# Kernel optimization log

Hardware: AMD Instinct MI355X
Metric: run time of the kernel (lower is better)

## Reference

```python
import jax, jax.numpy as jnp
import numpy as np

B, S, D, H = 4, 2048, 1024, 16
HD = D // H  # head_dim = 64


def rope(x):
    # canonical interleaved RoPE over the full feature dim, applied pre-head-split
    # x: [B, S, D]
    d = x.shape[-1]
    inv_freq = 1.0 / (10000.0 ** (jnp.arange(0, d, 2, dtype=jnp.float32) / d))  # [D/2]
    pos = jnp.arange(x.shape[1], dtype=jnp.float32)
    ang = pos[:, None] * inv_freq[None, :]          # [S, D/2]
    cos, sin = jnp.cos(ang), jnp.sin(ang)
    x1, x2 = x[..., 0::2], x[..., 1::2]             # even/odd pairs
    r1 = x1 * cos - x2 * sin
    r2 = x1 * sin + x2 * cos
    return jnp.stack([r1, r2], axis=-1).reshape(x.shape)


def setup_inputs() -> dict:
    key = jax.random.key(0)
    ks = jax.random.split(key, 9)
    s = 1.0 / np.sqrt(D)
    def lin(k):
        kw, kb = jax.random.split(k)
        W = jax.random.uniform(kw, (D, D), jnp.float32, -s, s)
        b = jax.random.uniform(kb, (D,), jnp.float32, -s, s)
        return W, b
    Wq, bq = lin(ks[0]); Wk, bk = lin(ks[1]); Wv, bv = lin(ks[2]); W0, b0 = lin(ks[3])
    x = jax.random.normal(ks[4], (B, S, D), jnp.float32)
    return {"x": x, "Wq": Wq, "bq": bq, "Wk": Wk, "bk": bk,
            "Wv": Wv, "bv": bv, "W0": W0, "b0": b0}


def reference(x, Wq, bq, Wk, bk, Wv, bv, W0, b0):
    # QKV projections (torch Linear: x @ W.T + b; here W stored as [in, out])
    q = x @ Wq + bq
    k = x @ Wk + bk
    v = x @ Wv + bv
    # RoPE applied to full d_model before head split (as in the source)
    q = rope(q)
    k = rope(k)
    # split heads -> [B, H, S, HD]
    b, s, _ = x.shape
    qh = q.reshape(b, s, H, HD).transpose(0, 2, 1, 3)
    kh = k.reshape(b, s, H, HD).transpose(0, 2, 1, 3)
    vh = v.reshape(b, s, H, HD).transpose(0, 2, 1, 3)
    scores = jnp.einsum("bhqd,bhkd->bhqk", qh, kh) / jnp.sqrt(jnp.float32(HD))
    attn = jax.nn.softmax(scores, axis=-1)  # dropout p=0.0 -> identity
    out = jnp.einsum("bhqk,bhkd->bhqd", attn, vh)
    out = out.transpose(0, 2, 1, 3).reshape(b, s, D)
    return out @ W0 + b0
```

## Files before the change

### kernel.cpp

```cpp
#include <hip/hip_runtime.h>
#include <hip/hip_bf16.h>

typedef unsigned short u16;
typedef u16 u16x8 __attribute__((ext_vector_type(8)));
typedef float f32x4 __attribute__((ext_vector_type(4)));
typedef __bf16 bf16x8 __attribute__((ext_vector_type(8)));

#define B_ 4
#define S_ 2048
#define D_ 1024
#define H_ 16
#define HD_ 64
#define M_ (B_*S_)

#if __has_builtin(__builtin_amdgcn_exp2f)
#define EXP2(x) __builtin_amdgcn_exp2f(x)
#else
#define EXP2(x) exp2f(x)
#endif

__device__ __forceinline__ f32x4 MFMA(u16x8 a, u16x8 b, f32x4 c) {
  return __builtin_amdgcn_mfma_f32_16x16x32_bf16(
      __builtin_bit_cast(bf16x8, a), __builtin_bit_cast(bf16x8, b), c, 0, 0, 0);
}

__device__ __forceinline__ u16 f2b(float f) {
  return __builtin_bit_cast(u16, __float2bfloat16(f));
}

__device__ __forceinline__ void load_lds16(const void* g, void* l) {
  __builtin_amdgcn_global_load_lds(
      (const __attribute__((address_space(1))) void*)g,
      (__attribute__((address_space(3))) void*)l, 16, 0, 0);
}

__device__ __forceinline__ unsigned int cvtpk(float lo, float hi) {
  unsigned int r;
  asm("v_cvt_pk_bf16_f32 %0, %1, %2" : "=v"(r) : "v"(lo), "v"(hi));
  return r;
}

__global__ __launch_bounds__(256) void k_rope_tab(float2* __restrict__ tab) {
  int i = blockIdx.x * 256 + threadIdx.x;
  if (i >= S_ * (D_ / 2)) return;
  int s = i >> 9;
  int f = i & 511;
  float invf = (float)exp(-(double)f / 512.0 * 9.210340371976184);
  float ang = (float)s * invf;
  tab[i] = make_float2(cosf(ang), sinf(ang));
}

__global__ __launch_bounds__(256) void k_cvt(const float* __restrict__ x,
                                             u16* __restrict__ xb, int n) {
  int i = blockIdx.x * 256 + threadIdx.x;
  if (i * 4 >= n) return;
  float4 v = ((const float4*)x)[i];
  ushort4 o;
  o.x = f2b(v.x); o.y = f2b(v.y); o.z = f2b(v.z); o.w = f2b(v.w);
  ((ushort4*)xb)[i] = o;
}

__global__ __launch_bounds__(256) void k_transpose4(
    const float* __restrict__ Wq, const float* __restrict__ Wk,
    const float* __restrict__ Wv, const float* __restrict__ W0,
    u16* __restrict__ Tq, u16* __restrict__ Tk, u16* __restrict__ Tv,
    u16* __restrict__ T0) {
  const float* W = (blockIdx.z == 0) ? Wq : (blockIdx.z == 1) ? Wk
                   : (blockIdx.z == 2) ? Wv : W0;
  u16* WT = (blockIdx.z == 0) ? Tq : (blockIdx.z == 1) ? Tk
            : (blockIdx.z == 2) ? Tv : T0;
  __shared__ float t[32][33];
  int tx = threadIdx.x, ty = threadIdx.y;
  int bx = blockIdx.x * 32, by = blockIdx.y * 32;
#pragma unroll
  for (int j = 0; j < 32; j += 8)
    t[ty + j][tx] = W[(size_t)(by + ty + j) * D_ + bx + tx];
  __syncthreads();
#pragma unroll
  for (int j = 0; j < 32; j += 8)
    WT[(size_t)(bx + ty + j) * D_ + by + tx] = f2b(t[tx][ty + j]);
}

template <int NM>
__global__ __launch_bounds__(512, 2) void k_gemm256(
    const u16* __restrict__ A, const u16* __restrict__ BT,
    const float* __restrict__ b0p, const float* __restrict__ b1p,
    const float* __restrict__ b2p, const float2* __restrict__ tab,
    u16* __restrict__ O0, u16* __restrict__ O1, u16* __restrict__ O2,
    float* __restrict__ FO) {
  __shared__ __attribute__((aligned(16))) u16 Al0[16384], Al1[16384];
  __shared__ __attribute__((aligned(16))) u16 Bl0[16384], Bl1[16384];
  const int tid = threadIdx.x;
  const int lane = tid & 63, wid = tid >> 6;
  const int wm = wid >> 2, wn = wid & 3;
  const int g = lane >> 4, c = lane & 15;
  const int flat = blockIdx.x;
  const int xcd = flat & 7, idx = flat >> 3;
  const int bx = xcd * 4 + (idx & 3), by = idx >> 2;
  const int rowbase = bx * 256;

  const int rr_ = tid >> 3, slot = tid & 7;
  const int sw8 = slot ^ (rr_ & 7);
  const u16* aB = A + (size_t)(rowbase + rr_) * 1024 + sw8 * 8;
  const u16* bB = BT + (size_t)(by * 256 + rr_) * 1024 + sw8 * 8;
  const int wdst = wid * 512;

  f32x4 acc[8][4] = {};
  const int swz = (c & 7) << 3;
  const int k0o = (g * 8) ^ swz;
  const int k1o = k0o ^ 32;
  const int ArdB = (wm * 128 + c) * 64;
  const int BrdB = (wn * 64 + c) * 64;

  u16x8 bf00, bf01, bf10, bf11, bf20, bf21, bf30, bf31;

#define ISSUE_LO(NA, NB, KT)                                                 \
  load_lds16(aB + (KT), &NA[wdst]);                                          \
  load_lds16(aB + 65536 + (KT), &NA[4096 + wdst]);                           \
  load_lds16(bB + (KT), &NB[wdst]);                                          \
  load_lds16(bB + 65536 + (KT), &NB[4096 + wdst]);
#define ISSUE_HI(NA, NB, KT)                                                 \
  load_lds16(aB + 131072 + (KT), &NA[8192 + wdst]);                          \
  load_lds16(aB + 196608 + (KT), &NA[12288 + wdst]);                         \
  load_lds16(bB + 131072 + (KT), &NB[8192 + wdst]);                          \
  load_lds16(bB + 196608 + (KT), &NB[12288 + wdst]);
#define PBAR                                                                 \
  __builtin_amdgcn_sched_barrier(0);                                         \
  __builtin_amdgcn_s_barrier();                                              \
  asm volatile("s_waitcnt lgkmcnt(0)" ::: "memory");                         \
  __builtin_amdgcn_sched_barrier(0);                                         \
  __builtin_amdgcn_s_setprio(1);
#define PEND                                                                 \
  __builtin_amdgcn_s_setprio(0);                                             \
  __builtin_amdgcn_sched_barrier(0);                                         \
  __builtin_amdgcn_s_barrier();
#define LDB8(CB)                                                             \
  bf00 = *(const u16x8*)&CB[BrdB + k0o];                                     \
  bf01 = *(const u16x8*)&CB[BrdB + k1o];                                     \
  bf10 = *(const u16x8*)&CB[BrdB + 1024 + k0o];                              \
  bf11 = *(const u16x8*)&CB[BrdB + 1024 + k1o];                              \
  bf20 = *(const u16x8*)&CB[BrdB + 2048 + k0o];                              \
  bf21 = *(const u16x8*)&CB[BrdB + 2048 + k1o];                              \
  bf30 = *(const u16x8*)&CB[BrdB + 3072 + k0o];                              \
  bf31 = *(const u16x8*)&CB[BrdB + 3072 + k1o];
#define LDA4(CA, MI0)                                                        \
  a00 = *(const u16x8*)&CA[ArdB + (MI0) * 1024 + k0o];                       \
  a01 = *(const u16x8*)&CA[ArdB + (MI0) * 1024 + k1o];                       \
  a10 = *(const u16x8*)&CA[ArdB + (MI0 + 1) * 1024 + k0o];                   \
  a11 = *(const u16x8*)&CA[ArdB + (MI0 + 1) * 1024 + k1o];
#define MFMA16(MI0)                                                          \
  acc[MI0][0] = MFMA(a00, bf00, acc[MI0][0]);                                \
  acc[MI0][0] = MFMA(a01, bf01, acc[MI0][0]);                                \
  acc[MI0][1] = MFMA(a00, bf10, acc[MI0][1]);                                \
  acc[MI0][1] = MFMA(a01, bf11, acc[MI0][1]);                                \
  acc[MI0][2] = MFMA(a00, bf20, acc[MI0][2]);                                \
  acc[MI0][2] = MFMA(a01, bf21, acc[MI0][2]);                                \
  acc[MI0][3] = MFMA(a00, bf30, acc[MI0][3]);                                \
  acc[MI0][3] = MFMA(a01, bf31, acc[MI0][3]);                                \
  acc[MI0 + 1][0] = MFMA(a10, bf00, acc[MI0 + 1][0]);                        \
  acc[MI0 + 1][0] = MFMA(a11, bf01, acc[MI0 + 1][0]);                        \
  acc[MI0 + 1][1] = MFMA(a10, bf10, acc[MI0 + 1][1]);                        \
  acc[MI0 + 1][1] = MFMA(a11, bf11, acc[MI0 + 1][1]);                        \
  acc[MI0 + 1][2] = MFMA(a10, bf20, acc[MI0 + 1][2]);                        \
  acc[MI0 + 1][2] = MFMA(a11, bf21, acc[MI0 + 1][2]);                        \
  acc[MI0 + 1][3] = MFMA(a10, bf30, acc[MI0 + 1][3]);                        \
  acc[MI0 + 1][3] = MFMA(a11, bf31, acc[MI0 + 1][3]);
#define TILE(CA, CB, NA, NB, KT, STG)                                        \
  {                                                                          \
    u16x8 a00, a01, a10, a11;                                                \
    if (STG) { ISSUE_LO(NA, NB, KT) }                                        \
    LDB8(CB) LDA4(CA, 0)                                                     \
    PBAR MFMA16(0) PEND                                                      \
    if (STG) { ISSUE_HI(NA, NB, KT) }                                        \
    LDA4(CA, 2) PBAR MFMA16(2) PEND                                          \
    LDA4(CA, 4) PBAR MFMA16(4) PEND                                          \
    LDA4(CA, 6) PBAR MFMA16(6)                                               \
    __builtin_amdgcn_s_setprio(0);                                           \
    __syncthreads();                                                         \
  }

  ISSUE_LO(Al0, Bl0, 0)
  ISSUE_HI(Al0, Bl0, 0)
  __syncthreads();

#pragma unroll 1
  for (int it = 0; it < 7; ++it) {
    const int kt1 = (2 * it + 1) * 64, kt2 = (2 * it + 2) * 64;
    TILE(Al0, Bl0, Al1, Bl1, kt1, 1)
    TILE(Al1, Bl1, Al0, Bl0, kt2, 1)
  }
  TILE(Al0, Bl0, Al1, Bl1, 15 * 64, 1)
  TILE(Al1, Bl1, Al0, Bl0, 0, 0)

  if (NM == 0) {
    const int mode = by >> 2;
    const float* bias = (mode == 0) ? b0p : (mode == 1) ? b1p : b2p;
    u16* Cout = (mode == 0) ? O0 : (mode == 1) ? O1 : O2;
    const int colL0 = (by & 3) * 256 + wn * 64;
    int coln[4];
    float bn[4];
#pragma unroll
    for (int ni = 0; ni < 4; ++ni) {
      coln[ni] = colL0 + ni * 16 + c;
      bn[ni] = bias[coln[ni]];
    }
    if (mode == 2) {
#pragma unroll
      for (int mi = 0; mi < 8; ++mi) {
        const int row0 = rowbase + wm * 128 + mi * 16 + g * 4;
        const int s0 = row0 & (S_ - 1);
        const int bidx = row0 >> 11;
#pragma unroll
        for (int ni = 0; ni < 4; ++ni) {
          const int h = coln[ni] >> 6, hd = coln[ni] & 63;
          ushort4 w;
          w.x = f2b(acc[mi][ni][0] + bn[ni]);
          w.y = f2b(acc[mi][ni][1] + bn[ni]);
          w.z = f2b(acc[mi][ni][2] + bn[ni]);
          w.w = f2b(acc[mi][ni][3] + bn[ni]);
          *(ushort4*)(Cout + ((size_t)(bidx * H_ + h) * HD_ + hd) * S_ + s0) = w;
        }
      }
    } else {
      const float qs = 0.18033688011112042f;
#pragma unroll
      for (int mi = 0; mi < 8; ++mi) {
#pragma unroll
        for (int rq = 0; rq < 4; ++rq) {
          const int row = rowbase + wm * 128 + mi * 16 + g * 4 + rq;
          const int s = row & (S_ - 1);
          const int bidx = row >> 11;
#pragma unroll
          for (int ni = 0; ni < 4; ++ni) {
            float v = acc[mi][ni][rq] + bn[ni];
            float2 cs = tab[(size_t)s * 512 + (coln[ni] >> 1)];
            float nb = __shfl_xor(v, 1);
            v = (lane & 1) ? (nb * cs.y + v * cs.x) : (v * cs.x - nb * cs.y);
            if (mode == 0) v *= qs;
            const int h = coln[ni] >> 6, hd = coln[ni] & 63;
            Cout[(((size_t)(bidx * H_ + h)) * S_ + s) * HD_ + hd] = f2b(v);
          }
        }
      }
    }
  } else {
    const int colb = by * 256 + wn * 64;
#pragma unroll
    for (int mi = 0; mi < 8; ++mi) {
#pragma unroll
      for (int rq = 0; rq < 4; ++rq) {
        const int row = rowbase + wm * 128 + mi * 16 + g * 4 + rq;
#pragma unroll
        for (int ni = 0; ni < 4; ++ni) {
          const int coln = colb + ni * 16 + c;
          FO[(size_t)row * D_ + coln] = acc[mi][ni][rq] + b0p[coln];
        }
      }
    }
  }
#undef TILE
#undef MFMA16
#undef LDA4
#undef LDB8
#undef PEND
#undef PBAR
#undef ISSUE_HI
#undef ISSUE_LO
}

__global__ __launch_bounds__(512, 4) void k_attn(const u16* __restrict__ Qh,
                                                 const u16* __restrict__ Kh,
                                                 const u16* __restrict__ Vt,
                                                 u16* __restrict__ AO) {
  __shared__ __attribute__((aligned(16))) u16 Kl0[4096], Kl1[4096];
  __shared__ __attribute__((aligned(16))) u16 Vl0[4096], Vl1[4096];
  __shared__ __attribute__((aligned(16))) u16 Pl[16384];
  const int tid = threadIdx.x;
  const int lane = tid & 63, wid = tid >> 6;
  const int g = lane >> 4, c = lane & 15;
  const int flat = blockIdx.x;
  const int swzid = (flat & 7) * 64 + (flat >> 3);
  const int bh = swzid >> 3, qt = swzid & 7;
  const size_t base = (size_t)bh * S_ * HD_;
  const int qr0 = qt * 256 + wid * 32;

  u16x8 qf[2][2];
#pragma unroll
  for (int qg = 0; qg < 2; ++qg)
#pragma unroll
    for (int ks = 0; ks < 2; ++ks)
      qf[qg][ks] = *(const u16x8*)(Qh + base +
                                   (size_t)(qr0 + qg * 16 + c) * HD_ +
                                   ks * 32 + g * 8);

  f32x4 o20[4] = {}, o21[4] = {};
  float L0 = 0.f, L1 = 0.f;

  const int swz = (c & 7) << 3;
  const int kb0 = c * 64 + ((g * 8) ^ swz);
  const int kb1 = c * 64 + ((32 + g * 8) ^ swz);
  const int pwA0 = wid * 2048 + ((c * 64 + 0 * 16 + g * 4) ^ swz);
  const int pwA1 = wid * 2048 + ((c * 64 + 1 * 16 + g * 4) ^ swz);
  const int pwA2 = wid * 2048 + ((c * 64 + 2 * 16 + g * 4) ^ swz);
  const int pwA3 = wid * 2048 + ((c * 64 + 3 * 16 + g * 4) ^ swz);
  const int pbA0 = wid * 2048 + kb0;
  const int pbA1 = wid * 2048 + kb1;
  const f32x4 z4 = {0.f, 0.f, 0.f, 0.f};

  const int ldrow = lane >> 3, ldslot = lane & 7;
  const int srow = wid * 8 + ldrow;
  const u16* kp0 = Kh + base + (size_t)srow * HD_ + (ldslot ^ (srow & 7)) * 8;
  const u16* vp0 = Vt + base + (size_t)srow * S_ + (ldslot ^ (srow & 7)) * 8;
  const int kdst0 = wid * 512;

#define STAGE(KP, VP)                                                        \
  {                                                                          \
    load_lds16(kp0, &KP[kdst0]); kp0 += 64 * HD_;                            \
    load_lds16(vp0, &VP[kdst0]); vp0 += 64;                                  \
  }

#define BODY(KC, VC, KP, VP)                                                 \
  {                                                                          \
    STAGE(KP, VP);                                                           \
    f32x4 s40[4], s41[4];                                                    \
    __builtin_amdgcn_s_setprio(1);                                           \
    _Pragma("unroll") for (int n = 0; n < 4; ++n) {                          \
      u16x8 kfa = *(const u16x8*)&KC[n * 1024 + kb0];                        \
      u16x8 kfb = *(const u16x8*)&KC[n * 1024 + kb1];                        \
      s40[n] = MFMA(kfa, qf[0][0], z4);                                      \
      s40[n] = MFMA(kfb, qf[0][1], s40[n]);                                  \
      s41[n] = MFMA(kfa, qf[1][0], z4);                                      \
      s41[n] = MFMA(kfb, qf[1][1], s41[n]);                                  \
    }                                                                        \
    __builtin_amdgcn_s_setprio(0);                                           \
    float rs0 = 0.f, rs1 = 0.f;                                              \
    _Pragma("unroll") for (int n = 0; n < 4; ++n) {                          \
      float p0[4], p1[4];                                                    \
      _Pragma("unroll") for (int r = 0; r < 4; ++r) {                        \
        p0[r] = EXP2(s40[n][r]); rs0 += p0[r];                               \
        p1[r] = EXP2(s41[n][r]); rs1 += p1[r];                               \
      }                                                                      \
      uint2 w0, w1;                                                          \
      w0.x = cvtpk(p0[0], p0[1]); w0.y = cvtpk(p0[2], p0[3]);                \
      w1.x = cvtpk(p1[0], p1[1]); w1.y = cvtpk(p1[2], p1[3]);                \
      const int pw = (n == 0) ? pwA0 : (n == 1) ? pwA1 : (n == 2) ? pwA2     \
                                                                  : pwA3;   \
      *(uint2*)&Pl[pw] = w0;                                                 \
      *(uint2*)&Pl[pw + 1024] = w1;                                          \
    }                                                                        \
    L0 += rs0; L1 += rs1;                                                    \
    asm volatile("s_waitcnt lgkmcnt(0)" ::: "memory");                       \
    __builtin_amdgcn_sched_barrier(0);                                       \
    __builtin_amdgcn_s_setprio(1);                                           \
    {                                                                        \
      u16x8 pa00 = *(const u16x8*)&Pl[pbA0];                                 \
      u16x8 pa01 = *(const u16x8*)&Pl[pbA1];                                 \
      u16x8 pa10 = *(const u16x8*)&Pl[pbA0 + 1024];                          \
      u16x8 pa11 = *(const u16x8*)&Pl[pbA1 + 1024];                          \
      _Pragma("unroll") for (int nd = 0; nd < 4; ++nd) {                     \
        u16x8 va0 = *(const u16x8*)&VC[nd * 1024 + kb0];                     \
        u16x8 va1 = *(const u16x8*)&VC[nd * 1024 + kb1];                     \
        o20[nd] = MFMA(va0, pa00, o20[nd]);                                  \
        o20[nd] = MFMA(va1, pa01, o20[nd]);                                  \
        o21[nd] = MFMA(va0, pa10, o21[nd]);                                  \
        o21[nd] = MFMA(va1, pa11, o21[nd]);                                  \
      }                                                                      \
    }                                                                        \
    __builtin_amdgcn_s_setprio(0);                                           \
    __syncthreads();                                                         \
  }

  STAGE(Kl0, Vl0);
  __syncthreads();

#pragma unroll 1
  for (int it = 0; it < 16; ++it) {
    BODY(Kl0, Vl0, Kl1, Vl1);
    BODY(Kl1, Vl1, Kl0, Vl0);
  }

  L0 += __shfl_xor(L0, 16);
  L0 += __shfl_xor(L0, 32);
  L1 += __shfl_xor(L1, 16);
  L1 += __shfl_xor(L1, 32);
  const float inv0 = 1.f / L0, inv1 = 1.f / L1;
  const int b = bh >> 4, h = bh & (H_ - 1);
#pragma unroll
  for (int nd = 0; nd < 4; ++nd) {
    ushort4 w;
    w.x = f2b(o20[nd][0] * inv0);
    w.y = f2b(o20[nd][1] * inv0);
    w.z = f2b(o20[nd][2] * inv0);
    w.w = f2b(o20[nd][3] * inv0);
    *(ushort4*)(AO + ((size_t)(b * S_ + qr0 + c)) * D_ + h * HD_ + nd * 16 +
                g * 4) = w;
    ushort4 w2;
    w2.x = f2b(o21[nd][0] * inv1);
    w2.y = f2b(o21[nd][1] * inv1);
    w2.z = f2b(o21[nd][2] * inv1);
    w2.w = f2b(o21[nd][3] * inv1);
    *(ushort4*)(AO + ((size_t)(b * S_ + qr0 + 16 + c)) * D_ + h * HD_ +
                nd * 16 + g * 4) = w2;
  }
#undef BODY
#undef STAGE
}

extern "C" void kernel_launch(void* const* d_in, const int* in_sizes, int n_in,
                              void* d_out, int out_size, void* d_ws,
                              size_t ws_size, hipStream_t stream) {
  const float* x  = (const float*)d_in[0];
  const float* Wq = (const float*)d_in[1];
  const float* bq = (const float*)d_in[2];
  const float* Wk = (const float*)d_in[3];
  const float* bk = (const float*)d_in[4];
  const float* Wv = (const float*)d_in[5];
  const float* bv = (const float*)d_in[6];
  const float* W0 = (const float*)d_in[7];
  const float* b0 = (const float*)d_in[8];
  float* out = (float*)d_out;

  char* ws = (char*)d_ws;
  const size_t MiB = (size_t)1 << 20;
  float2* tab = (float2*)(ws + 0);
  u16* xb  = (u16*)(ws + 8 * MiB);
  u16* WqT = (u16*)(ws + 24 * MiB);
  u16* WkT = (u16*)(ws + 26 * MiB);
  u16* WvT = (u16*)(ws + 28 * MiB);
  u16* W0T = (u16*)(ws + 30 * MiB);
  u16* Qh  = (u16*)(ws + 32 * MiB);
  u16* Kh  = (u16*)(ws + 48 * MiB);
  u16* Vt  = (u16*)(ws + 64 * MiB);
  u16* AO  = (u16*)(ws + 80 * MiB);

  k_rope_tab<<<4096, 256, 0, stream>>>(tab);
  k_cvt<<<(M_ * D_ / 4 + 255) / 256, 256, 0, stream>>>(x, xb, M_ * D_);
  k_transpose4<<<dim3(32, 32, 4), dim3(32, 8), 0, stream>>>(
      Wq, Wk, Wv, W0, WqT, WkT, WvT, W0T);
  k_gemm256<0><<<384, 512, 0, stream>>>(xb, WqT, bq, bk, bv, tab,
                                        Qh, Kh, Vt, nullptr);
  k_attn<<<512, 512, 0, stream>>>(Qh, Kh, Vt, AO);
  k_gemm256<1><<<128, 512, 0, stream>>>(AO, W0T, b0, nullptr, nullptr, nullptr,
                                        nullptr, nullptr, nullptr, out);
}
```

Measured before the change: 193.8 us.

## Replace output-projection 256x256 GEMM with 128x128 tile kernel for more blocks

The output projection previously reused the 256x256-tile pipelined GEMM, which launched only 128 blocks on a GPU with many more compute units. A new simple 128x128-tile GEMM (256 threads, 512 blocks) replaces it to fill more CUs, and the QKV GEMM template is de-templated. The RoPE table now uses a float exp2f instead of a double-precision exp. The new kernel lacks double buffering and an LDS swizzle, so it risks more bank conflicts and exposed load latency per tile.

```diff
diff --git a/kernel.cpp b/kernel.cpp
--- a/kernel.cpp
+++ b/kernel.cpp
@@ -45,7 +45,7 @@
   if (i >= S_ * (D_ / 2)) return;
   int s = i >> 9;
   int f = i & 511;
-  float invf = (float)exp(-(double)f / 512.0 * 9.210340371976184);
+  float invf = exp2f((float)f * (-13.287712379549449f / 512.0f));
   float ang = (float)s * invf;
   tab[i] = make_float2(cosf(ang), sinf(ang));
 }
@@ -81,13 +81,11 @@
     WT[(size_t)(bx + ty + j) * D_ + by + tx] = f2b(t[tx][ty + j]);
 }
 
-template <int NM>
-__global__ __launch_bounds__(512, 2) void k_gemm256(
+__global__ __launch_bounds__(512, 2) void k_gemm256_qkv(
     const u16* __restrict__ A, const u16* __restrict__ BT,
-    const float* __restrict__ b0p, const float* __restrict__ b1p,
-    const float* __restrict__ b2p, const float2* __restrict__ tab,
-    u16* __restrict__ O0, u16* __restrict__ O1, u16* __restrict__ O2,
-    float* __restrict__ FO) {
+    const float* __restrict__ bq, const float* __restrict__ bk,
+    const float* __restrict__ bv, const float2* __restrict__ tab,
+    u16* __restrict__ Qh, u16* __restrict__ Kh, u16* __restrict__ Vt) {
   __shared__ __attribute__((aligned(16))) u16 Al0[16384], Al1[16384];
   __shared__ __attribute__((aligned(16))) u16 Bl0[16384], Bl1[16384];
   const int tid = threadIdx.x;
@@ -192,68 +190,52 @@
   TILE(Al0, Bl0, Al1, Bl1, 15 * 64, 1)
   TILE(Al1, Bl1, Al0, Bl0, 0, 0)
 
-  if (NM == 0) {
-    const int mode = by >> 2;
-    const float* bias = (mode == 0) ? b0p : (mode == 1) ? b1p : b2p;
-    u16* Cout = (mode == 0) ? O0 : (mode == 1) ? O1 : O2;
-    const int colL0 = (by & 3) * 256 + wn * 64;
-    int coln[4];
-    float bn[4];
-#pragma unroll
-    for (int ni = 0; ni < 4; ++ni) {
-      coln[ni] = colL0 + ni * 16 + c;
-      bn[ni] = bias[coln[ni]];
-    }
-    if (mode == 2) {
-#pragma unroll
-      for (int mi = 0; mi < 8; ++mi) {
-        const int row0 = rowbase + wm * 128 + mi * 16 + g * 4;
-        const int s0 = row0 & (S_ - 1);
-        const int bidx = row0 >> 11;
-#pragma unroll
-        for (int ni = 0; ni < 4; ++ni) {
-          const int h = coln[ni] >> 6, hd = coln[ni] & 63;
-          ushort4 w;
-          w.x = f2b(acc[mi][ni][0] + bn[ni]);
-          w.y = f2b(acc[mi][ni][1] + bn[ni]);
-          w.z = f2b(acc[mi][ni][2] + bn[ni]);
-          w.w = f2b(acc[mi][ni][3] + bn[ni]);
-          *(ushort4*)(Cout + ((size_t)(bidx * H_ + h) * HD_ + hd) * S_ + s0) = w;
-        }
-      }
-    } else {
-      const float qs = 0.18033688011112042f;
-#pragma unroll
-      for (int mi = 0; mi < 8; ++mi) {
-#pragma unroll
-        for (int rq = 0; rq < 4; ++rq) {
-          const int row = rowbase + wm * 128 + mi * 16 + g * 4 + rq;
-          const int s = row & (S_ - 1);
-          const int bidx = row >> 11;
-#pragma unroll
-          for (int ni = 0; ni < 4; ++ni) {
-            float v = acc[mi][ni][rq] + bn[ni];
-            float2 cs = tab[(size_t)s * 512 + (coln[ni] >> 1)];
-            float nb = __shfl_xor(v, 1);
-            v = (lane & 1) ? (nb * cs.y + v * cs.x) : (v * cs.x - nb * cs.y);
-            if (mode == 0) v *= qs;
-            const int h = coln[ni] >> 6, hd = coln[ni] & 63;
-            Cout[(((size_t)(bidx * H_ + h)) * S_ + s) * HD_ + hd] = f2b(v);
-          }
-        }
+  const int mode = by >> 2;
+  const float* bias = (mode == 0) ? bq : (mode == 1) ? bk : bv;
+  u16* Cout = (mode == 0) ? Qh : (mode == 1) ? Kh : Vt;
+  const int colL0 = (by & 3) * 256 + wn * 64;
+  int coln[4];
+  float bn[4];
+#pragma unroll
+  for (int ni = 0; ni < 4; ++ni) {
+    coln[ni] = colL0 + ni * 16 + c;
+    bn[ni] = bias[coln[ni]];
+  }
+  if (mode == 2) {
+#pragma unroll
+    for (int mi = 0; mi < 8; ++mi) {
+      const int row0 = rowbase + wm * 128 + mi * 16 + g * 4;
+      const int s0 = row0 & (S_ - 1);
+      const int bidx = row0 >> 11;
+#pragma unroll
+      for (int ni = 0; ni < 4; ++ni) {
+        const int h = coln[ni] >> 6, hd = coln[ni] & 63;
+        ushort4 w;
+        w.x = f2b(acc[mi][ni][0] + bn[ni]);
+        w.y = f2b(acc[mi][ni][1] + bn[ni]);
+        w.z = f2b(acc[mi][ni][2] + bn[ni]);
+        w.w = f2b(acc[mi][ni][3] + bn[ni]);
+        *(ushort4*)(Cout + ((size_t)(bidx * H_ + h) * HD_ + hd) * S_ + s0) = w;
       }
     }
   } else {
-    const int colb = by * 256 + wn * 64;
+    const float qs = 0.18033688011112042f;
 #pragma unroll
     for (int mi = 0; mi < 8; ++mi) {
 #pragma unroll
       for (int rq = 0; rq < 4; ++rq) {
         const int row = rowbase + wm * 128 + mi * 16 + g * 4 + rq;
+        const int s = row & (S_ - 1);
+        const int bidx = row >> 11;
 #pragma unroll
         for (int ni = 0; ni < 4; ++ni) {
-          const int coln = colb + ni * 16 + c;
-          FO[(size_t)row * D_ + coln] = acc[mi][ni][rq] + b0p[coln];
+          float v = acc[mi][ni][rq] + bn[ni];
+          float2 cs = tab[(size_t)s * 512 + (coln[ni] >> 1)];
+          float nb = __shfl_xor(v, 1);
+          v = (lane & 1) ? (nb * cs.y + v * cs.x) : (v * cs.x - nb * cs.y);
+          if (mode == 0) v *= qs;
+          const int h = coln[ni] >> 6, hd = coln[ni] & 63;
+          Cout[(((size_t)(bidx * H_ + h)) * S_ + s) * HD_ + hd] = f2b(v);
         }
       }
     }
@@ -266,6 +248,69 @@
 #undef PBAR
 #undef ISSUE_HI
 #undef ISSUE_LO
+}
+
+__global__ __launch_bounds__(256, 2) void k_gemm_o(
+    const u16* __restrict__ A, const u16* __restrict__ BT,
+    const float* __restrict__ bias, float* __restrict__ Cout) {
+  __shared__ __attribute__((aligned(16))) u16 Al[128 * 64];
+  __shared__ __attribute__((aligned(16))) u16 Bl[128 * 64];
+  const int tid = threadIdx.x;
+  const int lane = tid & 63, wid = tid >> 6;
+  const int wr = wid >> 1, wc = wid & 1;
+  const int g = lane >> 4, c = lane & 15;
+  const int flat = blockIdx.y * gridDim.x + blockIdx.x;
+  const int xcd = flat & 7, idx = flat >> 3;
+  const int bx = xcd * 8 + (idx & 7), by = idx >> 3;
+  const int rowbase = bx * 128, colbase = by * 128;
+
+  f32x4 acc[4][4] = {};
+  const int ldr = lane >> 3;
+  const int ldk = (lane & 7) * 8;
+
+  for (int kt = 0; kt < D_; kt += 64) {
+    __syncthreads();
+#pragma unroll
+    for (int j = 0; j < 4; ++j) {
+      const int chunk = wid * 4 + j;
+      const int rr = chunk * 8 + ldr;
+      load_lds16(A + (size_t)(rowbase + rr) * D_ + kt + ldk, &Al[chunk * 512]);
+      load_lds16(BT + (size_t)(colbase + rr) * D_ + kt + ldk, &Bl[chunk * 512]);
+    }
+    __syncthreads();
+#pragma unroll
+    for (int ks = 0; ks < 2; ++ks) {
+      u16x8 a[4], b[4];
+#pragma unroll
+      for (int m = 0; m < 4; ++m)
+        a[m] = *(const u16x8*)&Al[(wr * 64 + m * 16 + c) * 64 + ks * 32 + g * 8];
+#pragma unroll
+      for (int n = 0; n < 4; ++n)
+        b[n] = *(const u16x8*)&Bl[(wc * 64 + n * 16 + c) * 64 + ks * 32 + g * 8];
+#pragma unroll
+      for (int m = 0; m < 4; ++m)
+#pragma unroll
+        for (int n = 0; n < 4; ++n)
+          acc[m][n] = MFMA(a[m], b[n], acc[m][n]);
+    }
+  }
+
+  int coln[4];
+  float bn[4];
+#pragma unroll
+  for (int n = 0; n < 4; ++n) {
+    coln[n] = colbase + wc * 64 + n * 16 + c;
+    bn[n] = bias[coln[n]];
+  }
+#pragma unroll
+  for (int m = 0; m < 4; ++m)
+#pragma unroll
+    for (int r = 0; r < 4; ++r) {
+      const int row = rowbase + wr * 64 + m * 16 + g * 4 + r;
+#pragma unroll
+      for (int n = 0; n < 4; ++n)
+        Cout[(size_t)row * D_ + coln[n]] = acc[m][n][r] + bn[n];
+    }
 }
 
 __global__ __launch_bounds__(512, 4) void k_attn(const u16* __restrict__ Qh,
@@ -437,9 +482,7 @@
   k_cvt<<<(M_ * D_ / 4 + 255) / 256, 256, 0, stream>>>(x, xb, M_ * D_);
   k_transpose4<<<dim3(32, 32, 4), dim3(32, 8), 0, stream>>>(
       Wq, Wk, Wv, W0, WqT, WkT, WvT, W0T);
-  k_gemm256<0><<<384, 512, 0, stream>>>(xb, WqT, bq, bk, bv, tab,
-                                        Qh, Kh, Vt, nullptr);
+  k_gemm256_qkv<<<384, 512, 0, stream>>>(xb, WqT, bq, bk, bv, tab, Qh, Kh, Vt);
   k_attn<<<512, 512, 0, stream>>>(Qh, Kh, Vt, AO);
-  k_gemm256<1><<<128, 512, 0, stream>>>(AO, W0T, b0, nullptr, nullptr, nullptr,
-                                        nullptr, nullptr, nullptr, out);
-}
+  k_gemm_o<<<dim3(64, 8), 256, 0, stream>>>(AO, W0T, b0, out);
+}
```

New measurement: 191.5 us. About the same (-1.2%).
